# Kernel tuning notes

Measured on AMD Instinct MI355X. Metric: run time of the kernel, lower is better.

## Reference

```python
import jax, jax.numpy as jnp
import numpy as np

B, K, D = 8, 4000, 256
H, DQ, DV = 8, 32, 32
WIN, PAD = 200, 50
STEP = WIN - 2 * PAD  # 100
BETA = 0.25


def setup_inputs() -> dict:
    key = jax.random.key(0)
    ks = jax.random.split(key, 14)
    s = 0.02
    return {
        "query": jax.random.normal(ks[0], (B, K, D), jnp.float32),
        "key": jax.random.normal(ks[1], (B, K, D), jnp.float32),
        "value": jax.random.normal(ks[2], (B, K, D), jnp.float32),
        "Wq": jax.random.normal(ks[3], (D, H * DQ), jnp.float32) * s,
        "bq": jax.random.normal(ks[4], (H * DQ,), jnp.float32) * s,
        "Wk": jax.random.normal(ks[5], (D, H * DQ), jnp.float32) * s,
        "bk": jax.random.normal(ks[6], (H * DQ,), jnp.float32) * s,
        "Wv": jax.random.normal(ks[7], (D, H * DV), jnp.float32) * s,
        "bv": jax.random.normal(ks[8], (H * DV,), jnp.float32) * s,
        "Wo": jax.random.normal(ks[9], (H * DV, D), jnp.float32) * s,
        "bo": jax.random.normal(ks[10], (D,), jnp.float32) * s,
    }


def _windows(x, n_win):
    starts = jnp.arange(n_win) * STEP
    idx = starts[:, None] + jnp.arange(WIN)[None, :]
    return x[:, :, idx, :]


def reference(query, key, value, Wq, bq, Wk, bk, Wv, bv, Wo, bo):
    b, k_len, d = query.shape
    pad = lambda t: jnp.pad(t, ((0, 0), (PAD, PAD), (0, 0)), mode='edge')  # replicate pad
    qp, kp, vp = pad(query), pad(key), pad(value)
    kpad = k_len + 2 * PAD
    n_win = (kpad - WIN) // STEP + 1

    def proj(x, Wm, bias, dh):
        y = x @ Wm + bias                       # [B, Kp, H*dh]
        return y.reshape(b, kpad, H, dh).transpose(0, 2, 1, 3)  # [B, H, Kp, dh]

    q = _windows(proj(qp, Wq, bq, DQ), n_win)
    kk = _windows(proj(kp, Wk, bk, DQ), n_win)
    v = _windows(proj(vp, Wv, bv, DV), n_win)

    scores = jnp.einsum('bhnid,bhnjd->bhnij', q, kk) / jnp.sqrt(jnp.float32(WIN))
    dist = jnp.abs(jnp.arange(WIN)[:, None] - jnp.arange(WIN)[None, :]).astype(scores.dtype)
    cauchy = (1.0 / (1.0 + BETA * dist * dist)) * (1.0 - jnp.eye(WIN, dtype=scores.dtype))
    scores = scores * cauchy
    causal = jnp.triu(jnp.ones((WIN, WIN), dtype=bool), k=1)  # attention_size is not None -> causal masking
    scores = jnp.where(causal, -jnp.inf, scores)
    attn = jax.nn.softmax(scores, axis=-1)
    out = jnp.einsum('bhnij,bhnjd->bhnid', attn, v)
    out = out[:, :, :, PAD:WIN - PAD, :].reshape(b, H, k_len, DV)
    out = out.transpose(0, 2, 1, 3).reshape(b, k_len, H * DV)  # heads concatenated, head-major slices
    return out @ Wo + bo
```

## Files before the change

kernel.cpp:

```cpp
#include <hip/hip_runtime.h>


typedef __bf16 bf16_t;
typedef __bf16 bf16x4 __attribute__((ext_vector_type(4)));
typedef __bf16 bf16x8 __attribute__((ext_vector_type(8)));
typedef float  f32x4  __attribute__((ext_vector_type(4)));

#define MFMA16(a, b, c) __builtin_amdgcn_mfma_f32_16x16x32_bf16((a), (b), (c), 0, 0, 0)

static __device__ __forceinline__ bf16x4 cvt4(float4 a) {
  bf16x4 r;
  r[0] = (bf16_t)a.x; r[1] = (bf16_t)a.y; r[2] = (bf16_t)a.z; r[3] = (bf16_t)a.w;
  return r;
}

static __device__ __forceinline__ unsigned short bbits(bf16_t v) {
  union { bf16_t b; unsigned short u; } c; c.b = v; return c.u;
}

__global__ __launch_bounds__(256)
void prep_weights(const float* __restrict__ Wq, const float* __restrict__ Wk,
                  const float* __restrict__ Wv, const float* __restrict__ Wo,
                  bf16_t* __restrict__ wt) {
  const int mat  = blockIdx.x >> 6;
  const int tile = blockIdx.x & 63;
  const int kt = (tile >> 3) * 32, nt = (tile & 7) * 32;
  const float* W = (mat == 0) ? Wq : (mat == 1) ? Wk : (mat == 2) ? Wv : Wo;
  __shared__ float t[32][33];
  const int tx = threadIdx.x & 31, ty = threadIdx.x >> 5;
#pragma unroll
  for (int i = 0; i < 32; i += 8)
    t[ty + i][tx] = W[(size_t)(kt + ty + i) * 256 + nt + tx];
  __syncthreads();
  bf16_t* dst = wt + (size_t)mat * 65536;
#pragma unroll
  for (int i = 0; i < 32; i += 8)
    dst[(size_t)(nt + ty + i) * 256 + kt + tx] = (bf16_t)t[tx][ty + i];
}

template <int MODE>
__global__ __launch_bounds__(512)
void gemm256(const void* __restrict__ Xv, const bf16_t* __restrict__ Wt,
             const float* __restrict__ bias, void* __restrict__ Out, int M,
             float oscale = 1.f) {
  constexpr bool INB = (MODE == 3);
  const int m0 = blockIdx.x * 64;
  __shared__ bf16_t la[64 * 40];
  __shared__ bf16_t lb[256 * 40];
  const int tid  = threadIdx.x;
  const int lane = tid & 63;
  const int wv   = tid >> 6;
  const int wm   = (wv & 3) * 16;
  const int wn   = (wv >> 2) * 128;
  const int lo   = lane & 15, hi = lane >> 4;
  int ar = m0 + (tid >> 3); if (ar >= M) ar = M - 1;

  f32x4 acc[8] = {};

  for (int kk = 0; kk < 256; kk += 32) {
    if constexpr (!INB) {
      const float* X = (const float*)Xv + (size_t)ar * 256 + kk + (tid & 7) * 4;
      *(bf16x4*)&la[(tid >> 3) * 40 + (tid & 7) * 4] = cvt4(*(const float4*)X);
    } else {
      const bf16_t* X = (const bf16_t*)Xv + (size_t)ar * 256 + kk + (tid & 7) * 4;
      *(bf16x4*)&la[(tid >> 3) * 40 + (tid & 7) * 4] = *(const bf16x4*)X;
    }
    {
      const bf16_t* Wp = Wt + (size_t)(tid >> 1) * 256 + kk + (tid & 1) * 16;
      bf16_t* dst = &lb[(tid >> 1) * 40 + (tid & 1) * 16];
      *(bf16x8*)dst       = ((const bf16x8*)Wp)[0];
      *(bf16x8*)(dst + 8) = ((const bf16x8*)Wp)[1];
    }
    __syncthreads();

    const bf16x8 af = *(const bf16x8*)&la[(wm + lo) * 40 + hi * 8];
#pragma unroll
    for (int ni = 0; ni < 8; ++ni) {
      const bf16x8 bfv = *(const bf16x8*)&lb[(wn + ni * 16 + lo) * 40 + hi * 8];
      acc[ni] = MFMA16(af, bfv, acc[ni]);
    }
    __syncthreads();
  }

#pragma unroll
  for (int ni = 0; ni < 8; ++ni) {
    const int n   = wn + ni * 16 + lo;
    const float bia = bias[n];
    const int mb  = m0 + wm + hi * 4;
    if (mb >= M) continue;
    if constexpr (MODE == 0) {
      bf16_t* O = (bf16_t*)Out;
#pragma unroll
      for (int r = 0; r < 4; ++r)
        O[(size_t)(mb + r) * 256 + n] = (bf16_t)((acc[ni][r] + bia) * oscale);
    } else if constexpr (MODE == 1) {
      const int b = mb / 4000, t = mb - b * 4000;
      bf16_t* O = (bf16_t*)Out;
#pragma unroll
      for (int r = 0; r < 4; ++r)
        O[((size_t)b * 4064 + t + 50 + r) * 256 + n] = (bf16_t)(acc[ni][r] + bia);
    } else if constexpr (MODE == 2) {
      const int b = mb / 4000, t = mb - b * 4000;
      const int h = n >> 5, dv = n & 31;
      bf16_t* O = (bf16_t*)Out + ((size_t)((b * 8 + h) * 32 + dv)) * 4064 + t + 50;
      unsigned short e0 = bbits((bf16_t)(acc[ni][0] + bia));
      unsigned short e1 = bbits((bf16_t)(acc[ni][1] + bia));
      unsigned short e2 = bbits((bf16_t)(acc[ni][2] + bia));
      unsigned short e3 = bbits((bf16_t)(acc[ni][3] + bia));
      unsigned* O32 = (unsigned*)O;
      O32[0] = (unsigned)e0 | ((unsigned)e1 << 16);
      O32[1] = (unsigned)e2 | ((unsigned)e3 << 16);
    } else {
      float* O = (float*)Out;
#pragma unroll
      for (int r = 0; r < 4; ++r)
        O[(size_t)(mb + r) * 256 + n] = acc[ni][r] + bia;
    }
  }
}

__global__ void fill_edges(bf16_t* __restrict__ kb, bf16_t* __restrict__ vt, int nb) {
  const int idx = blockIdx.x * 256 + threadIdx.x;
  const int kcnt = nb * 64 * 256;
  if (idx < kcnt) {
    const int b  = idx >> 14;
    const int pp = (idx >> 8) & 63;
    const int nn = idx & 255;
    const int p  = (pp < 50) ? pp : pp + 4000;
    bf16_t v = (pp < 50) ? kb[((size_t)b * 4064 + 50) * 256 + nn] : (bf16_t)0.f;
    kb[((size_t)b * 4064 + p) * 256 + nn] = v;
  } else {
    const int j  = idx - kcnt;
    const int bh = j >> 11;
    const int dv = (j >> 6) & 31;
    const int pp = j & 63;
    const int p  = (pp < 50) ? pp : pp + 4000;
    bf16_t v = (pp < 50) ? vt[((size_t)bh * 32 + dv) * 4064 + 50] : (bf16_t)0.f;
    vt[((size_t)bh * 32 + dv) * 4064 + p] = v;
  }
}

__global__ __launch_bounds__(448)
void attn_win(const bf16_t* __restrict__ qb, const bf16_t* __restrict__ kb,
              const bf16_t* __restrict__ vt, bf16_t* __restrict__ ao) {
  const int blk = blockIdx.x;
  const int n = blk % 40;
  const int h = (blk / 40) & 7;
  const int b = blk / 320;
  const int wv = threadIdx.x >> 6;
  const int lane = threadIdx.x & 63;
  const int lo = lane & 15, hi = lane >> 4;

  __shared__ __align__(16) bf16_t E[7][16][40];

  const int i0 = 50 + 16 * wv;
  int jtmax = (65 + 16 * wv) >> 4;
  if (jtmax > 9) jtmax = 9;
  const int reach = jtmax * 16 + 16;

  int tq = n * 100 + 16 * wv + lo;
  if (tq > 3999) tq = 3999;
  const bf16x8 qf = *(const bf16x8*)&qb[((size_t)b * 4000 + tq) * 256 + h * 32 + hi * 8];

  const f32x4 zero = {0.f, 0.f, 0.f, 0.f};
  bf16x8 onesf;
#pragma unroll
  for (int u = 0; u < 8; ++u) onesf[u] = (bf16_t)1.0f;

  f32x4 o0 = zero, o1 = zero, sm = zero;
  const size_t vbase = ((size_t)((b * 8 + h) * 32)) * 4064 + n * 100;
  const size_t kbase = ((size_t)(b * 4064 + n * 100)) * 256 + h * 32 + hi * 8;
  const int dbase = i0 + hi * 4 - lo;

#pragma unroll
  for (int kt = 0; kt < 5; ++kt) if (kt * 32 < reach) {
#pragma unroll
    for (int half = 0; half < 2; ++half) {
      const int jt = kt * 2 + half;
      if (jt <= jtmax) {
        const bf16x8 kf = *(const bf16x8*)&kb[kbase + (size_t)(jt * 16 + lo) * 256];
        const f32x4 s = MFMA16(qf, kf, zero);
#pragma unroll
        for (int r = 0; r < 4; ++r) {
          const int d = dbase + r - jt * 16;
          const float df = (float)d;
          float c = __builtin_amdgcn_rcpf(__builtin_fmaf(0.25f * df, df, 1.f));
          c = (d == 0) ? 0.f : c;
          float e = __expf(s[r] * c);
          e = (d < 0) ? 0.f : e;
          E[wv][hi * 4 + r][half * 16 + lo] = (bf16_t)e;
        }
      } else {
#pragma unroll
        for (int r = 0; r < 4; ++r)
          E[wv][hi * 4 + r][half * 16 + lo] = (bf16_t)0.f;
      }
    }
    const bf16x8 pf = *(const bf16x8*)&E[wv][lo][hi * 8];
    const bf16x8 v0 = *(const bf16x8*)&vt[vbase + (size_t)lo * 4064 + kt * 32 + hi * 8];
    const bf16x8 v1 = *(const bf16x8*)&vt[vbase + (size_t)(16 + lo) * 4064 + kt * 32 + hi * 8];
    o0 = MFMA16(pf, v0, o0);
    o1 = MFMA16(pf, v1, o1);
    sm = MFMA16(pf, onesf, sm);
  }

#pragma unroll
  for (int r = 0; r < 4; ++r) {
    const int i = i0 + hi * 4 + r;
    if (i < 150) {
      const float ri = __builtin_amdgcn_rcpf(sm[r]);
      const int t = n * 100 + i - 50;
      bf16_t* op = &ao[((size_t)b * 4000 + t) * 256 + h * 32];
      op[lo]      = (bf16_t)(o0[r] * ri);
      op[16 + lo] = (bf16_t)(o1[r] * ri);
    }
  }
}

extern "C" void kernel_launch(void* const* d_in, const int* in_sizes, int n_in,
                              void* d_out, int out_size, void* d_ws, size_t ws_size,
                              hipStream_t stream) {
  (void)in_sizes; (void)n_in; (void)out_size;
  const float* query = (const float*)d_in[0];
  const float* key   = (const float*)d_in[1];
  const float* value = (const float*)d_in[2];
  const float* Wq = (const float*)d_in[3];
  const float* bq = (const float*)d_in[4];
  const float* Wk = (const float*)d_in[5];
  const float* bk = (const float*)d_in[6];
  const float* Wv = (const float*)d_in[7];
  const float* bv = (const float*)d_in[8];
  const float* Wo = (const float*)d_in[9];
  const float* bo = (const float*)d_in[10];

  int bc = 8;
  while (bc > 1 && 524288ull + (unsigned long long)bc * 8257536ull > (unsigned long long)ws_size)
    bc >>= 1;

  bf16_t* wt = (bf16_t*)d_ws;
  bf16_t* qb = wt + 4 * 65536;
  bf16_t* kb = qb + (size_t)bc * 4000 * 256;
  bf16_t* vt = kb + (size_t)bc * 4064 * 256;
  bf16_t* ao = vt + (size_t)bc * 8 * 32 * 4064;

  prep_weights<<<256, 256, 0, stream>>>(Wq, Wk, Wv, Wo, wt);

  const float qscale = 0.07071067811865475f;

  for (int b0 = 0; b0 < 8; b0 += bc) {
    const int M = bc * 4000;
    const int mblk = (M + 63) / 64;
    const float* qx = query + (size_t)b0 * 4000 * 256;
    const float* kx = key   + (size_t)b0 * 4000 * 256;
    const float* vx = value + (size_t)b0 * 4000 * 256;
    float* ox = (float*)d_out + (size_t)b0 * 4000 * 256;

    gemm256<0><<<dim3(mblk), 512, 0, stream>>>(qx, wt + 0 * 65536, bq, qb, M, qscale);
    gemm256<1><<<dim3(mblk), 512, 0, stream>>>(kx, wt + 1 * 65536, bk, kb, M, 1.f);
    gemm256<2><<<dim3(mblk), 512, 0, stream>>>(vx, wt + 2 * 65536, bv, vt, M, 1.f);
    fill_edges<<<bc * 128, 256, 0, stream>>>(kb, vt, bc);
    attn_win<<<bc * 320, 448, 0, stream>>>(qb, kb, vt, ao);
    gemm256<3><<<dim3(mblk), 512, 0, stream>>>(ao, wt + 3 * 65536, bo, ox, M, 1.f);
  }
}
```

Baseline: 106.2 us.

## Restructure projection GEMMs: full-weight LDS staging, register A tiles, merged QKV launch

```diff
diff --git a/kernel.cpp b/kernel.cpp
--- a/kernel.cpp
+++ b/kernel.cpp
@@ -2,15 +2,15 @@
 
 
 typedef __bf16 bf16_t;
-typedef __bf16 bf16x4 __attribute__((ext_vector_type(4)));
 typedef __bf16 bf16x8 __attribute__((ext_vector_type(8)));
 typedef float  f32x4  __attribute__((ext_vector_type(4)));
 
 #define MFMA16(a, b, c) __builtin_amdgcn_mfma_f32_16x16x32_bf16((a), (b), (c), 0, 0, 0)
 
-static __device__ __forceinline__ bf16x4 cvt4(float4 a) {
-  bf16x4 r;
+static __device__ __forceinline__ bf16x8 cvt8(float4 a, float4 b) {
+  bf16x8 r;
   r[0] = (bf16_t)a.x; r[1] = (bf16_t)a.y; r[2] = (bf16_t)a.z; r[3] = (bf16_t)a.w;
+  r[4] = (bf16_t)b.x; r[5] = (bf16_t)b.y; r[6] = (bf16_t)b.z; r[7] = (bf16_t)b.w;
   return r;
 }
 
@@ -38,71 +38,77 @@
     dst[(size_t)(nt + ty + i) * 256 + kt + tx] = (bf16_t)t[tx][ty + i];
 }
 
-template <int MODE>
+static __device__ __forceinline__ void stage_B(const bf16_t* __restrict__ W,
+                                               bf16_t* lb, int tid) {
+#pragma unroll
+  for (int i = 0; i < 16; ++i) {
+    const int g    = tid + i * 512;
+    const int row  = g >> 5;
+    const int colb = (g & 31) << 4;
+    const bf16x8 w = *(const bf16x8*)&W[row * 256 + (colb >> 1)];
+    *(bf16x8*)((char*)lb + row * 512 + (colb ^ ((row & 7) << 4))) = w;
+  }
+}
+
 __global__ __launch_bounds__(512)
-void gemm256(const void* __restrict__ Xv, const bf16_t* __restrict__ Wt,
-             const float* __restrict__ bias, void* __restrict__ Out, int M,
-             float oscale = 1.f) {
-  constexpr bool INB = (MODE == 3);
-  const int m0 = blockIdx.x * 64;
-  __shared__ bf16_t la[64 * 40];
-  __shared__ bf16_t lb[256 * 40];
-  const int tid  = threadIdx.x;
-  const int lane = tid & 63;
-  const int wv   = tid >> 6;
-  const int wm   = (wv & 3) * 16;
-  const int wn   = (wv >> 2) * 128;
-  const int lo   = lane & 15, hi = lane >> 4;
-  int ar = m0 + (tid >> 3); if (ar >= M) ar = M - 1;
-
-  f32x4 acc[8] = {};
-
-  for (int kk = 0; kk < 256; kk += 32) {
-    if constexpr (!INB) {
-      const float* X = (const float*)Xv + (size_t)ar * 256 + kk + (tid & 7) * 4;
-      *(bf16x4*)&la[(tid >> 3) * 40 + (tid & 7) * 4] = cvt4(*(const float4*)X);
+void proj_gemm(const float* __restrict__ qx, const float* __restrict__ kx,
+               const float* __restrict__ vx, const bf16_t* __restrict__ wt,
+               const float* __restrict__ bq, const float* __restrict__ bk,
+               const float* __restrict__ bv,
+               bf16_t* __restrict__ qb, bf16_t* __restrict__ kb,
+               bf16_t* __restrict__ vt, int M, float qscale) {
+  const int mode = blockIdx.y;
+  const float* X    = (mode == 0) ? qx : (mode == 1) ? kx : vx;
+  const float* bias = (mode == 0) ? bq : (mode == 1) ? bk : bv;
+
+  __shared__ bf16_t lb[65536];
+  const int tid = threadIdx.x;
+  stage_B(wt + (size_t)mode * 65536, lb, tid);
+
+  const int lane = tid & 63, wv = tid >> 6;
+  const int lo = lane & 15, hi = lane >> 4;
+  const int m0 = blockIdx.x * 128;
+  int ar = m0 + wv * 16 + lo; if (ar >= M) ar = M - 1;
+
+  bf16x8 areg[8];
+#pragma unroll
+  for (int kk = 0; kk < 8; ++kk) {
+    const float* ap = X + (size_t)ar * 256 + kk * 32 + hi * 8;
+    areg[kk] = cvt8(((const float4*)ap)[0], ((const float4*)ap)[1]);
+  }
+  __syncthreads();
+
+  f32x4 acc[16] = {};
+#pragma unroll
+  for (int kk = 0; kk < 8; ++kk) {
+#pragma unroll
+    for (int ni = 0; ni < 16; ++ni) {
+      const int row = ni * 16 + lo;
+      const int off = row * 512 + (((kk * 64) + hi * 16) ^ ((row & 7) << 4));
+      const bf16x8 bfrag = *(const bf16x8*)((const char*)lb + off);
+      acc[ni] = MFMA16(areg[kk], bfrag, acc[ni]);
+    }
+  }
+
+  const int mb = m0 + wv * 16 + hi * 4;
+  if (mb >= M) return;
+#pragma unroll
+  for (int ni = 0; ni < 16; ++ni) {
+    const int n = ni * 16 + lo;
+    const float bia = bias[n];
+    if (mode == 0) {
+#pragma unroll
+      for (int r = 0; r < 4; ++r)
+        qb[(size_t)(mb + r) * 256 + n] = (bf16_t)((acc[ni][r] + bia) * qscale);
+    } else if (mode == 1) {
+      const int b = mb / 4000, t = mb - b * 4000;
+#pragma unroll
+      for (int r = 0; r < 4; ++r)
+        kb[((size_t)b * 4064 + t + 50 + r) * 256 + n] = (bf16_t)(acc[ni][r] + bia);
     } else {
-      const bf16_t* X = (const bf16_t*)Xv + (size_t)ar * 256 + kk + (tid & 7) * 4;
-      *(bf16x4*)&la[(tid >> 3) * 40 + (tid & 7) * 4] = *(const bf16x4*)X;
-    }
-    {
-      const bf16_t* Wp = Wt + (size_t)(tid >> 1) * 256 + kk + (tid & 1) * 16;
-      bf16_t* dst = &lb[(tid >> 1) * 40 + (tid & 1) * 16];
-      *(bf16x8*)dst       = ((const bf16x8*)Wp)[0];
-      *(bf16x8*)(dst + 8) = ((const bf16x8*)Wp)[1];
-    }
-    __syncthreads();
-
-    const bf16x8 af = *(const bf16x8*)&la[(wm + lo) * 40 + hi * 8];
-#pragma unroll
-    for (int ni = 0; ni < 8; ++ni) {
-      const bf16x8 bfv = *(const bf16x8*)&lb[(wn + ni * 16 + lo) * 40 + hi * 8];
-      acc[ni] = MFMA16(af, bfv, acc[ni]);
-    }
-    __syncthreads();
-  }
-
-#pragma unroll
-  for (int ni = 0; ni < 8; ++ni) {
-    const int n   = wn + ni * 16 + lo;
-    const float bia = bias[n];
-    const int mb  = m0 + wm + hi * 4;
-    if (mb >= M) continue;
-    if constexpr (MODE == 0) {
-      bf16_t* O = (bf16_t*)Out;
-#pragma unroll
-      for (int r = 0; r < 4; ++r)
-        O[(size_t)(mb + r) * 256 + n] = (bf16_t)((acc[ni][r] + bia) * oscale);
-    } else if constexpr (MODE == 1) {
-      const int b = mb / 4000, t = mb - b * 4000;
-      bf16_t* O = (bf16_t*)Out;
-#pragma unroll
-      for (int r = 0; r < 4; ++r)
-        O[((size_t)b * 4064 + t + 50 + r) * 256 + n] = (bf16_t)(acc[ni][r] + bia);
-    } else if constexpr (MODE == 2) {
       const int b = mb / 4000, t = mb - b * 4000;
       const int h = n >> 5, dv = n & 31;
-      bf16_t* O = (bf16_t*)Out + ((size_t)((b * 8 + h) * 32 + dv)) * 4064 + t + 50;
+      bf16_t* O = vt + ((size_t)((b * 8 + h) * 32 + dv)) * 4064 + t + 50;
       unsigned short e0 = bbits((bf16_t)(acc[ni][0] + bia));
       unsigned short e1 = bbits((bf16_t)(acc[ni][1] + bia));
       unsigned short e2 = bbits((bf16_t)(acc[ni][2] + bia));
@@ -110,12 +116,49 @@
       unsigned* O32 = (unsigned*)O;
       O32[0] = (unsigned)e0 | ((unsigned)e1 << 16);
       O32[1] = (unsigned)e2 | ((unsigned)e3 << 16);
-    } else {
-      float* O = (float*)Out;
-#pragma unroll
-      for (int r = 0; r < 4; ++r)
-        O[(size_t)(mb + r) * 256 + n] = acc[ni][r] + bia;
-    }
+    }
+  }
+}
+
+__global__ __launch_bounds__(512)
+void out_gemm(const bf16_t* __restrict__ ao, const bf16_t* __restrict__ wt,
+              const float* __restrict__ bias, float* __restrict__ Out, int M) {
+  __shared__ bf16_t lb[65536];
+  const int tid = threadIdx.x;
+  stage_B(wt, lb, tid);
+
+  const int lane = tid & 63, wv = tid >> 6;
+  const int lo = lane & 15, hi = lane >> 4;
+  const int m0 = blockIdx.x * 128;
+  int ar = m0 + wv * 16 + lo; if (ar >= M) ar = M - 1;
+
+  bf16x8 areg[8];
+#pragma unroll
+  for (int kk = 0; kk < 8; ++kk)
+    areg[kk] = *(const bf16x8*)&ao[(size_t)ar * 256 + kk * 32 + hi * 8];
+  __syncthreads();
+
+  f32x4 acc[16] = {};
+#pragma unroll
+  for (int kk = 0; kk < 8; ++kk) {
+#pragma unroll
+    for (int ni = 0; ni < 16; ++ni) {
+      const int row = ni * 16 + lo;
+      const int off = row * 512 + (((kk * 64) + hi * 16) ^ ((row & 7) << 4));
+      const bf16x8 bfrag = *(const bf16x8*)((const char*)lb + off);
+      acc[ni] = MFMA16(areg[kk], bfrag, acc[ni]);
+    }
+  }
+
+  const int mb = m0 + wv * 16 + hi * 4;
+  if (mb >= M) return;
+#pragma unroll
+  for (int ni = 0; ni < 16; ++ni) {
+    const int n = ni * 16 + lo;
+    const float bia = bias[n];
+#pragma unroll
+    for (int r = 0; r < 4; ++r)
+      Out[(size_t)(mb + r) * 256 + n] = acc[ni][r] + bia;
   }
 }
 
@@ -249,17 +292,16 @@
 
   for (int b0 = 0; b0 < 8; b0 += bc) {
     const int M = bc * 4000;
-    const int mblk = (M + 63) / 64;
+    const int mblk = (M + 127) / 128;
     const float* qx = query + (size_t)b0 * 4000 * 256;
     const float* kx = key   + (size_t)b0 * 4000 * 256;
     const float* vx = value + (size_t)b0 * 4000 * 256;
     float* ox = (float*)d_out + (size_t)b0 * 4000 * 256;
 
-    gemm256<0><<<dim3(mblk), 512, 0, stream>>>(qx, wt + 0 * 65536, bq, qb, M, qscale);
-    gemm256<1><<<dim3(mblk), 512, 0, stream>>>(kx, wt + 1 * 65536, bk, kb, M, 1.f);
-    gemm256<2><<<dim3(mblk), 512, 0, stream>>>(vx, wt + 2 * 65536, bv, vt, M, 1.f);
+    proj_gemm<<<dim3(mblk, 3), 512, 0, stream>>>(qx, kx, vx, wt, bq, bk, bv,
+                                                 qb, kb, vt, M, qscale);
     fill_edges<<<bc * 128, 256, 0, stream>>>(kb, vt, bc);
     attn_win<<<bc * 320, 448, 0, stream>>>(qb, kb, vt, ao);
-    gemm256<3><<<dim3(mblk), 512, 0, stream>>>(ao, wt + 3 * 65536, bo, ox, M, 1.f);
-  }
-}
+    out_gemm<<<dim3(mblk), 512, 0, stream>>>(ao, wt + 3 * 65536, bo, ox, M);
+  }
+}
```

After: 105.2 us. Within noise of the previous version (-1.0%).

## Double-buffer weight tiles via direct global-to-LDS loads and fuse edge padding into GEMMs

Applied to the files above, without the earlier changes.

```diff
diff --git a/kernel.cpp b/kernel.cpp
--- a/kernel.cpp
+++ b/kernel.cpp
@@ -2,15 +2,22 @@
 
 
 typedef __bf16 bf16_t;
-typedef __bf16 bf16x4 __attribute__((ext_vector_type(4)));
 typedef __bf16 bf16x8 __attribute__((ext_vector_type(8)));
 typedef float  f32x4  __attribute__((ext_vector_type(4)));
 
 #define MFMA16(a, b, c) __builtin_amdgcn_mfma_f32_16x16x32_bf16((a), (b), (c), 0, 0, 0)
 
-static __device__ __forceinline__ bf16x4 cvt4(float4 a) {
-  bf16x4 r;
+typedef __attribute__((address_space(1))) const unsigned char gas_u8;
+typedef __attribute__((address_space(3))) unsigned char las_u8;
+
+static __device__ __forceinline__ void gload16(const void* g, void* l) {
+  __builtin_amdgcn_global_load_lds((gas_u8*)g, (las_u8*)l, 16, 0, 0);
+}
+
+static __device__ __forceinline__ bf16x8 cvt8(float4 a, float4 b) {
+  bf16x8 r;
   r[0] = (bf16_t)a.x; r[1] = (bf16_t)a.y; r[2] = (bf16_t)a.z; r[3] = (bf16_t)a.w;
+  r[4] = (bf16_t)b.x; r[5] = (bf16_t)b.y; r[6] = (bf16_t)b.z; r[7] = (bf16_t)b.w;
   return r;
 }
 
@@ -40,103 +47,119 @@
 
 template <int MODE>
 __global__ __launch_bounds__(512)
-void gemm256(const void* __restrict__ Xv, const bf16_t* __restrict__ Wt,
-             const float* __restrict__ bias, void* __restrict__ Out, int M,
-             float oscale = 1.f) {
+void gemm5(const void* __restrict__ Xv, const bf16_t* __restrict__ W,
+           const float* __restrict__ bias, void* __restrict__ Out, int M,
+           float oscale) {
   constexpr bool INB = (MODE == 3);
-  const int m0 = blockIdx.x * 64;
-  __shared__ bf16_t la[64 * 40];
-  __shared__ bf16_t lb[256 * 40];
+  __shared__ __align__(16) char ldsB[2 * 16384];
+
   const int tid  = threadIdx.x;
   const int lane = tid & 63;
-  const int wv   = tid >> 6;
-  const int wm   = (wv & 3) * 16;
-  const int wn   = (wv >> 2) * 128;
+  const int w    = tid >> 6;
+  const int wm   = (w & 3) * 16;
+  const int wn   = (w >> 2) * 128;
   const int lo   = lane & 15, hi = lane >> 4;
-  int ar = m0 + (tid >> 3); if (ar >= M) ar = M - 1;
+  const int m0   = blockIdx.x * 64;
+
+  int ar = m0 + wm + lo; if (ar >= M) ar = M - 1;
+  bf16x8 areg[8];
+  if constexpr (!INB) {
+    const float4* ap = (const float4*)((const float*)Xv + (size_t)ar * 256);
+#pragma unroll
+    for (int t = 0; t < 8; ++t)
+      areg[t] = cvt8(ap[t * 8 + hi * 2], ap[t * 8 + hi * 2 + 1]);
+  } else {
+    const bf16_t* ap = (const bf16_t*)Xv + (size_t)ar * 256;
+#pragma unroll
+    for (int t = 0; t < 8; ++t)
+      areg[t] = *(const bf16x8*)(ap + t * 32 + hi * 8);
+  }
+
+  const bf16_t* bsrc[2];
+  int boff[2];
+#pragma unroll
+  for (int j = 0; j < 2; ++j) {
+    const int s = j * 512 + tid;
+    bsrc[j] = W + (size_t)(s >> 2) * 256 + ((s & 3) << 3);
+    boff[j] = s * 16;
+  }
+  int bbase[8];
+#pragma unroll
+  for (int ni = 0; ni < 8; ++ni)
+    bbase[ni] = (wn + ni * 16 + lo) * 64 + hi * 16;
+
+#pragma unroll
+  for (int j = 0; j < 2; ++j) gload16(bsrc[j], ldsB + boff[j]);
 
   f32x4 acc[8] = {};
 
-  for (int kk = 0; kk < 256; kk += 32) {
-    if constexpr (!INB) {
-      const float* X = (const float*)Xv + (size_t)ar * 256 + kk + (tid & 7) * 4;
-      *(bf16x4*)&la[(tid >> 3) * 40 + (tid & 7) * 4] = cvt4(*(const float4*)X);
+  for (int t = 0; t < 8; ++t) {
+    const int cur = (t & 1) * 16384;
+    if (t < 7) {
+      const int nxt = ((t + 1) & 1) * 16384;
+#pragma unroll
+      for (int j = 0; j < 2; ++j) gload16(bsrc[j] + (t + 1) * 32, ldsB + nxt + boff[j]);
+      asm volatile("s_waitcnt vmcnt(2)" ::: "memory");
     } else {
-      const bf16_t* X = (const bf16_t*)Xv + (size_t)ar * 256 + kk + (tid & 7) * 4;
-      *(bf16x4*)&la[(tid >> 3) * 40 + (tid & 7) * 4] = *(const bf16x4*)X;
-    }
-    {
-      const bf16_t* Wp = Wt + (size_t)(tid >> 1) * 256 + kk + (tid & 1) * 16;
-      bf16_t* dst = &lb[(tid >> 1) * 40 + (tid & 1) * 16];
-      *(bf16x8*)dst       = ((const bf16x8*)Wp)[0];
-      *(bf16x8*)(dst + 8) = ((const bf16x8*)Wp)[1];
-    }
-    __syncthreads();
-
-    const bf16x8 af = *(const bf16x8*)&la[(wm + lo) * 40 + hi * 8];
+      asm volatile("s_waitcnt vmcnt(0)" ::: "memory");
+    }
+    __builtin_amdgcn_sched_barrier(0);
+    __builtin_amdgcn_s_barrier();
+
 #pragma unroll
     for (int ni = 0; ni < 8; ++ni) {
-      const bf16x8 bfv = *(const bf16x8*)&lb[(wn + ni * 16 + lo) * 40 + hi * 8];
-      acc[ni] = MFMA16(af, bfv, acc[ni]);
-    }
-    __syncthreads();
-  }
-
+      const bf16x8 bfv = *(const bf16x8*)(ldsB + cur + bbase[ni]);
+      acc[ni] = MFMA16(areg[t], bfv, acc[ni]);
+    }
+    __builtin_amdgcn_sched_barrier(0);
+    __builtin_amdgcn_s_barrier();
+  }
+
+  const int mb = m0 + wm + hi * 4;
+  if (mb >= M) return;
 #pragma unroll
   for (int ni = 0; ni < 8; ++ni) {
-    const int n   = wn + ni * 16 + lo;
+    const int n = wn + ni * 16 + lo;
     const float bia = bias[n];
-    const int mb  = m0 + wm + hi * 4;
-    if (mb >= M) continue;
     if constexpr (MODE == 0) {
       bf16_t* O = (bf16_t*)Out;
 #pragma unroll
-      for (int r = 0; r < 4; ++r)
-        O[(size_t)(mb + r) * 256 + n] = (bf16_t)((acc[ni][r] + bia) * oscale);
+      for (int rr = 0; rr < 4; ++rr)
+        O[(size_t)(mb + rr) * 256 + n] = (bf16_t)((acc[ni][rr] + bia) * oscale);
     } else if constexpr (MODE == 1) {
       const int b = mb / 4000, t = mb - b * 4000;
       bf16_t* O = (bf16_t*)Out;
 #pragma unroll
-      for (int r = 0; r < 4; ++r)
-        O[((size_t)b * 4064 + t + 50 + r) * 256 + n] = (bf16_t)(acc[ni][r] + bia);
+      for (int rr = 0; rr < 4; ++rr) {
+        const bf16_t v = (bf16_t)(acc[ni][rr] + bia);
+        O[((size_t)b * 4064 + t + 50 + rr) * 256 + n] = v;
+        if (t == 0 && rr == 0)
+          for (int p = 0; p < 50; ++p)
+            O[((size_t)b * 4064 + p) * 256 + n] = v;
+      }
     } else if constexpr (MODE == 2) {
       const int b = mb / 4000, t = mb - b * 4000;
-      const int h = n >> 5, dv = n & 31;
-      bf16_t* O = (bf16_t*)Out + ((size_t)((b * 8 + h) * 32 + dv)) * 4064 + t + 50;
+      const size_t vrow = ((size_t)(b * 256 + n)) * 4064;
+      bf16_t* O = (bf16_t*)Out;
       unsigned short e0 = bbits((bf16_t)(acc[ni][0] + bia));
       unsigned short e1 = bbits((bf16_t)(acc[ni][1] + bia));
       unsigned short e2 = bbits((bf16_t)(acc[ni][2] + bia));
       unsigned short e3 = bbits((bf16_t)(acc[ni][3] + bia));
-      unsigned* O32 = (unsigned*)O;
+      unsigned* O32 = (unsigned*)(O + vrow + t + 50);
       O32[0] = (unsigned)e0 | ((unsigned)e1 << 16);
       O32[1] = (unsigned)e2 | ((unsigned)e3 << 16);
+      if (t == 0) {
+        const unsigned vv = (unsigned)e0 | ((unsigned)e0 << 16);
+        unsigned* P = (unsigned*)(O + vrow);
+#pragma unroll
+        for (int p = 0; p < 25; ++p) P[p] = vv;
+      }
     } else {
       float* O = (float*)Out;
 #pragma unroll
-      for (int r = 0; r < 4; ++r)
-        O[(size_t)(mb + r) * 256 + n] = acc[ni][r] + bia;
-    }
-  }
-}
-
-__global__ void fill_edges(bf16_t* __restrict__ kb, bf16_t* __restrict__ vt, int nb) {
-  const int idx = blockIdx.x * 256 + threadIdx.x;
-  const int kcnt = nb * 64 * 256;
-  if (idx < kcnt) {
-    const int b  = idx >> 14;
-    const int pp = (idx >> 8) & 63;
-    const int nn = idx & 255;
-    const int p  = (pp < 50) ? pp : pp + 4000;
-    bf16_t v = (pp < 50) ? kb[((size_t)b * 4064 + 50) * 256 + nn] : (bf16_t)0.f;
-    kb[((size_t)b * 4064 + p) * 256 + nn] = v;
-  } else {
-    const int j  = idx - kcnt;
-    const int bh = j >> 11;
-    const int dv = (j >> 6) & 31;
-    const int pp = j & 63;
-    const int p  = (pp < 50) ? pp : pp + 4000;
-    bf16_t v = (pp < 50) ? vt[((size_t)bh * 32 + dv) * 4064 + 50] : (bf16_t)0.f;
-    vt[((size_t)bh * 32 + dv) * 4064 + p] = v;
+      for (int rr = 0; rr < 4; ++rr)
+        O[(size_t)(mb + rr) * 256 + n] = acc[ni][rr] + bia;
+    }
   }
 }
 
@@ -168,7 +191,7 @@
   for (int u = 0; u < 8; ++u) onesf[u] = (bf16_t)1.0f;
 
   f32x4 o0 = zero, o1 = zero, sm = zero;
-  const size_t vbase = ((size_t)((b * 8 + h) * 32)) * 4064 + n * 100;
+  const size_t vbase = ((size_t)(b * 256 + h * 32)) * 4064 + n * 100;
   const size_t kbase = ((size_t)(b * 4064 + n * 100)) * 256 + h * 32 + hi * 8;
   const int dbase = i0 + hi * 4 - lo;
 
@@ -241,7 +264,7 @@
   bf16_t* qb = wt + 4 * 65536;
   bf16_t* kb = qb + (size_t)bc * 4000 * 256;
   bf16_t* vt = kb + (size_t)bc * 4064 * 256;
-  bf16_t* ao = vt + (size_t)bc * 8 * 32 * 4064;
+  bf16_t* ao = vt + (size_t)bc * 256 * 4064;
 
   prep_weights<<<256, 256, 0, stream>>>(Wq, Wk, Wv, Wo, wt);
 
@@ -255,11 +278,10 @@
     const float* vx = value + (size_t)b0 * 4000 * 256;
     float* ox = (float*)d_out + (size_t)b0 * 4000 * 256;
 
-    gemm256<0><<<dim3(mblk), 512, 0, stream>>>(qx, wt + 0 * 65536, bq, qb, M, qscale);
-    gemm256<1><<<dim3(mblk), 512, 0, stream>>>(kx, wt + 1 * 65536, bk, kb, M, 1.f);
-    gemm256<2><<<dim3(mblk), 512, 0, stream>>>(vx, wt + 2 * 65536, bv, vt, M, 1.f);
-    fill_edges<<<bc * 128, 256, 0, stream>>>(kb, vt, bc);
+    gemm5<0><<<mblk, 512, 0, stream>>>(qx, wt + 0 * 65536, bq, qb, M, qscale);
+    gemm5<1><<<mblk, 512, 0, stream>>>(kx, wt + 1 * 65536, bk, kb, M, 1.f);
+    gemm5<2><<<mblk, 512, 0, stream>>>(vx, wt + 2 * 65536, bv, vt, M, 1.f);
     attn_win<<<bc * 320, 448, 0, stream>>>(qb, kb, vt, ao);
-    gemm256<3><<<dim3(mblk), 512, 0, stream>>>(ao, wt + 3 * 65536, bo, ox, M, 1.f);
-  }
-}
+    gemm5<3><<<mblk, 512, 0, stream>>>(ao, wt + 3 * 65536, bo, ox, M, 1.f);
+  }
+}
```

After: 114.7 us. +8.1%, slower.
